# Performance work log

Hardware: AMD Instinct MI355X
Metric: run time of the kernel (lower is better)

The kernel has to match this reference:

```python
import jax, jax.numpy as jnp
import numpy as np

N = 100000      # nodes
E = 1600000     # edges (avg degree 16)
IN_DIM = 128
OUT_DIM = 64


def setup_inputs() -> dict:
    key = jax.random.key(0)
    k1, k2, k3, k4, k5 = jax.random.split(key, 5)
    h = jax.random.normal(k1, (N, IN_DIM), dtype=jnp.float32)
    W = jax.random.normal(k2, (IN_DIM, OUT_DIM), dtype=jnp.float32) * 0.05
    a = jax.random.normal(k3, (2 * OUT_DIM,), dtype=jnp.float32) * 0.05
    src = jax.random.randint(k4, (E,), 0, N, dtype=jnp.int32)
    dst = jax.random.randint(k5, (E,), 0, N, dtype=jnp.int32)
    return {"h": h, "W": W, "a": a, "src": src, "dst": dst}


def reference(h, W, a, src, dst):
    # z = W h  (node projection)
    z = h @ W                                   # [N, D]
    # Edge attention: e_ij = leaky_relu(a^T [z_i || z_j])
    # decomposed: a = [a_src; a_dst] -> e = leaky_relu(<z_src,a_src>+<z_dst,a_dst>)
    a_src, a_dst = a[:OUT_DIM], a[OUT_DIM:]
    s_src = z @ a_src                           # [N]
    s_dst = z @ a_dst                           # [N]
    e = jax.nn.leaky_relu(s_src[src] + s_dst[dst])  # [E], slope 0.01 (torch default)
    # Segmented softmax over incoming edges of each dst node
    m = jax.ops.segment_max(e, dst, num_segments=N)       # [N]
    m = jnp.where(jnp.isneginf(m), 0.0, m)                # empty mailboxes
    ex = jnp.exp(e - m[dst])                              # [E]
    denom = jax.ops.segment_sum(ex, dst, num_segments=N)  # [N]
    alpha = ex / jnp.where(denom == 0.0, 1.0, denom)[dst] # [E]
    # Weighted sum of source messages per dst node
    out = jax.ops.segment_sum(alpha[:, None] * z[src], dst, num_segments=N)  # [N, D]
    return out
```

## Files before the change

kernel.cpp:

```cpp
#include <hip/hip_runtime.h>
#include <math.h>

#define NN   100000
#define NE   1600000
#define IND  128
#define OUTD 64

#define BK_NODES 50
#define NBUCK    2000
#define CAPB     1024
#define CAPN     64

#define OFF_Z      0
#define OFF_SSRC   (OFF_Z + NN * OUTD / 2)
#define OFF_SDST   (OFF_SSRC + NN)
#define OFF_BCNT   (OFF_SDST + NN)
#define OFF_WSW    (OFF_BCNT + NBUCK)
#define OFF_COARSE (OFF_WSW + 4096)

typedef __bf16 bf16x8 __attribute__((ext_vector_type(8)));
typedef unsigned short u16x8 __attribute__((ext_vector_type(8)));
typedef float f32x4 __attribute__((ext_vector_type(4)));

union FragU { u16x8 u; bf16x8 b; };

__device__ __forceinline__ unsigned short f32_to_bf16_rne(float x)
{
    unsigned int b = __float_as_uint(x);
    b += 0x7FFFu + ((b >> 16) & 1u);
    return (unsigned short)(b >> 16);
}

#define WLPAD 136
#define ZTPAD 72

__global__ void __launch_bounds__(256) k_zs(
    const float* __restrict__ h, const unsigned short* __restrict__ wsw,
    const float* __restrict__ a, unsigned short* __restrict__ z16,
    float* __restrict__ s_src, float* __restrict__ s_dst)
{
    __shared__ __attribute__((aligned(16))) unsigned short HL[64 * WLPAD];
    int t = threadIdx.x;
    int base = blockIdx.x * 64;

    const float4* hg = reinterpret_cast<const float4*>(h);
#pragma unroll
    for (int i = 0; i < 8; ++i) {
        int idx = i * 256 + t;
        int r = idx >> 5;
        int c4 = idx & 31;
        float4 v = make_float4(0.f, 0.f, 0.f, 0.f);
        if (base + r < NN) v = hg[(base + r) * 32 + c4];
        unsigned int lo = (unsigned int)f32_to_bf16_rne(v.x) |
                          ((unsigned int)f32_to_bf16_rne(v.y) << 16);
        unsigned int hi = (unsigned int)f32_to_bf16_rne(v.z) |
                          ((unsigned int)f32_to_bf16_rne(v.w) << 16);
        *reinterpret_cast<uint2*>(&HL[r * WLPAD + c4 * 4]) = make_uint2(lo, hi);
    }

    int lane = t & 63;
    int wave = t >> 6;
    int c = lane & 15;
    int g = lane >> 4;

    FragU bf[4][4];
#pragma unroll
    for (int ks = 0; ks < 4; ++ks)
#pragma unroll
        for (int nt = 0; nt < 4; ++nt)
            bf[ks][nt].u = *reinterpret_cast<const u16x8*>(
                &wsw[((ks * 4 + nt) * 64 + lane) * 8]);

    __syncthreads();

    FragU af[4];
#pragma unroll
    for (int ks = 0; ks < 4; ++ks)
        af[ks].u = *reinterpret_cast<const u16x8*>(
            &HL[(wave * 16 + c) * WLPAD + ks * 32 + g * 8]);

    f32x4 acc[4];
#pragma unroll
    for (int nt = 0; nt < 4; ++nt) acc[nt] = (f32x4){0.f, 0.f, 0.f, 0.f};

#pragma unroll
    for (int nt = 0; nt < 4; ++nt)
#pragma unroll
        for (int ks = 0; ks < 4; ++ks)
            acc[nt] = __builtin_amdgcn_mfma_f32_16x16x32_bf16(
                af[ks].b, bf[ks][nt].b, acc[nt], 0, 0, 0);

    int rbase = base + wave * 16;
    float as[4], ad[4];
#pragma unroll
    for (int nt = 0; nt < 4; ++nt) {
        as[nt] = a[nt * 16 + c];
        ad[nt] = a[OUTD + nt * 16 + c];
    }

#pragma unroll
    for (int reg = 0; reg < 4; ++reg) {
        int row = rbase + g * 4 + reg;
        float p1 = 0.f, p2 = 0.f;
#pragma unroll
        for (int nt = 0; nt < 4; ++nt) {
            float v = acc[nt][reg];
            p1 = fmaf(v, as[nt], p1);
            p2 = fmaf(v, ad[nt], p2);
        }
#pragma unroll
        for (int mm = 1; mm < 16; mm <<= 1) {
            p1 += __shfl_xor(p1, mm, 64);
            p2 += __shfl_xor(p2, mm, 64);
        }
        if (c == 0 && row < NN) {
            s_src[row] = p1;
            s_dst[row] = p2;
        }
    }

    __syncthreads();
    unsigned short* ZT = HL;
    int zrow = wave * 16 + g * 4;
#pragma unroll
    for (int reg = 0; reg < 4; ++reg)
#pragma unroll
        for (int nt = 0; nt < 4; ++nt)
            ZT[(zrow + reg) * ZTPAD + nt * 16 + c] = f32_to_bf16_rne(acc[nt][reg]);
    __syncthreads();

#pragma unroll
    for (int i = 0; i < 2; ++i) {
        int j = i * 256 + t;
        int r = j >> 3;
        int c16 = j & 7;
        if (base + r < NN) {
            uint4 v = *reinterpret_cast<const uint4*>(&ZT[r * ZTPAD + c16 * 8]);
            *reinterpret_cast<uint4*>(&z16[(base + r) * OUTD + c16 * 8]) = v;
        }
    }
}

#define BIN_THREADS 1024
#define BIN_EPT     4
#define BIN_BLOCKS  391

__global__ void __launch_bounds__(BIN_THREADS) k_bin(
    const int* __restrict__ src, const int* __restrict__ dst,
    const float* __restrict__ W, unsigned short* __restrict__ wsw,
    int* __restrict__ bcnt, unsigned int* __restrict__ coarse)
{
    __shared__ int lhist[NBUCK];
    __shared__ int lbase[NBUCK];
    int t = threadIdx.x;

    if (blockIdx.x == 0) {
        int ks = t >> 8;
        int nt = (t >> 6) & 3;
        int lane = t & 63;
        int g = lane >> 4, c = lane & 15;
        u16x8 u;
#pragma unroll
        for (int j = 0; j < 8; ++j)
            u[j] = f32_to_bf16_rne(W[(ks * 32 + g * 8 + j) * OUTD + nt * 16 + c]);
        *reinterpret_cast<u16x8*>(&wsw[((ks * 4 + nt) * 64 + lane) * 8]) = u;
    }

    for (int i = t; i < NBUCK; i += BIN_THREADS) lhist[i] = 0;
    __syncthreads();

    int sv[BIN_EPT], dv[BIN_EPT];
    bool val[BIN_EPT];
#pragma unroll
    for (int i = 0; i < BIN_EPT; ++i) {
        int e = blockIdx.x * (BIN_THREADS * BIN_EPT) + i * BIN_THREADS + t;
        val[i] = e < NE;
        sv[i] = 0; dv[i] = 0;
        if (val[i]) { sv[i] = src[e]; dv[i] = dst[e]; }
    }
#pragma unroll
    for (int i = 0; i < BIN_EPT; ++i)
        if (val[i]) atomicAdd(&lhist[dv[i] / BK_NODES], 1);
    __syncthreads();

    for (int i = t; i < NBUCK; i += BIN_THREADS) {
        int c = lhist[i];
        lbase[i] = c ? atomicAdd(&bcnt[i], c) : 0;
        lhist[i] = 0;
    }
    __syncthreads();

#pragma unroll
    for (int i = 0; i < BIN_EPT; ++i) {
        if (val[i]) {
            int b = dv[i] / BK_NODES;
            int dl = dv[i] - b * BK_NODES;
            int r = atomicAdd(&lhist[b], 1);
            coarse[b * CAPB + lbase[b] + r] =
                ((unsigned int)sv[i] << 6) | (unsigned int)dl;
        }
    }
}

__global__ void __launch_bounds__(256) k_node(
    const unsigned short* __restrict__ z16, const unsigned int* __restrict__ coarse,
    const int* __restrict__ bcnt, const float* __restrict__ s_src,
    const float* __restrict__ s_dst, float* __restrict__ out)
{
    __shared__ unsigned int seg[BK_NODES * CAPN];
    __shared__ int cnt[BK_NODES];
    int b = blockIdx.x;
    int t = threadIdx.x;

    if (t < BK_NODES) cnt[t] = 0;
    __syncthreads();

    int nb = bcnt[b];
    if (nb > CAPB) nb = CAPB;
    const unsigned int* cb = coarse + b * CAPB;
    for (int i = t; i < nb; i += 256) {
        unsigned int v = cb[i];
        int dl = (int)(v & 63u);
        int s  = (int)(v >> 6);
        int r = atomicAdd(&cnt[dl], 1);
        if (r < CAPN) seg[dl * CAPN + r] = s;
    }
    __syncthreads();

    int wave = t >> 6;
    int lane = t & 63;
    int eslot = lane >> 4;
    int cbase = (lane & 15) * 4;

    for (int ni = wave; ni < BK_NODES; ni += 8) {
        int nj = ni + 4;
        bool hasB = (nj < BK_NODES);
        int nodeA = b * BK_NODES + ni;
        int nodeB = hasB ? (b * BK_NODES + nj) : nodeA;
        int dA = cnt[ni]; if (dA > CAPN) dA = CAPN;
        int dB = hasB ? cnt[nj] : 0; if (dB > CAPN) dB = CAPN;

        float sdstA = s_dst[nodeA];
        float sdstB = s_dst[nodeB];

        int sidA = 0, sidB = 0;
        float exA = 0.f, exB = 0.f;
        if (lane < dA) {
            sidA = (int)seg[ni * CAPN + lane];
            float e0 = s_src[sidA] + sdstA;
            exA = __expf(e0 > 0.f ? e0 : 0.01f * e0);
        }
        if (lane < dB) {
            sidB = (int)seg[nj * CAPN + lane];
            float e1 = s_src[sidB] + sdstB;
            exB = __expf(e1 > 0.f ? e1 : 0.01f * e1);
        }

        float lA = exA, lB = exB;
#pragma unroll
        for (int mm = 32; mm; mm >>= 1) {
            lA += __shfl_xor(lA, mm, 64);
            lB += __shfl_xor(lB, mm, 64);
        }
        int roA = sidA * OUTD;
        int roB = sidB * OUTD;

        float a0 = 0.f, a1 = 0.f, a2 = 0.f, a3 = 0.f;
        float c0 = 0.f, c1 = 0.f, c2 = 0.f, c3 = 0.f;
        int dmax = dA > dB ? dA : dB;
#pragma unroll 2
        for (int tt = 0; tt < dmax; tt += 4) {
            int e = tt + eslot;
            if (tt < dA) {
                int ro = __shfl(roA, e, 64);
                float exv = __shfl(exA, e, 64);
                uint2 v = *reinterpret_cast<const uint2*>(z16 + ro + cbase);
                a0 = fmaf(exv, __uint_as_float(v.x << 16), a0);
                a1 = fmaf(exv, __uint_as_float(v.x & 0xFFFF0000u), a1);
                a2 = fmaf(exv, __uint_as_float(v.y << 16), a2);
                a3 = fmaf(exv, __uint_as_float(v.y & 0xFFFF0000u), a3);
            }
            if (tt < dB) {
                int ro = __shfl(roB, e, 64);
                float exv = __shfl(exB, e, 64);
                uint2 v = *reinterpret_cast<const uint2*>(z16 + ro + cbase);
                c0 = fmaf(exv, __uint_as_float(v.x << 16), c0);
                c1 = fmaf(exv, __uint_as_float(v.x & 0xFFFF0000u), c1);
                c2 = fmaf(exv, __uint_as_float(v.y << 16), c2);
                c3 = fmaf(exv, __uint_as_float(v.y & 0xFFFF0000u), c3);
            }
        }

        a0 += __shfl_xor(a0, 16, 64); c0 += __shfl_xor(c0, 16, 64);
        a1 += __shfl_xor(a1, 16, 64); c1 += __shfl_xor(c1, 16, 64);
        a2 += __shfl_xor(a2, 16, 64); c2 += __shfl_xor(c2, 16, 64);
        a3 += __shfl_xor(a3, 16, 64); c3 += __shfl_xor(c3, 16, 64);
        a0 += __shfl_xor(a0, 32, 64); c0 += __shfl_xor(c0, 32, 64);
        a1 += __shfl_xor(a1, 32, 64); c1 += __shfl_xor(c1, 32, 64);
        a2 += __shfl_xor(a2, 32, 64); c2 += __shfl_xor(c2, 32, 64);
        a3 += __shfl_xor(a3, 32, 64); c3 += __shfl_xor(c3, 32, 64);

        if (eslot == 0) {
            float invA = dA ? 1.f / lA : 0.f;
            *reinterpret_cast<float4*>(out + nodeA * OUTD + cbase) =
                make_float4(a0 * invA, a1 * invA, a2 * invA, a3 * invA);
            if (hasB) {
                float invB = dB ? 1.f / lB : 0.f;
                *reinterpret_cast<float4*>(out + nodeB * OUTD + cbase) =
                    make_float4(c0 * invB, c1 * invB, c2 * invB, c3 * invB);
            }
        }
    }
}

extern "C" void kernel_launch(void* const* d_in, const int* in_sizes, int n_in,
                              void* d_out, int out_size, void* d_ws, size_t ws_size,
                              hipStream_t stream)
{
    const float* h   = (const float*)d_in[0];
    const float* W   = (const float*)d_in[1];
    const float* a   = (const float*)d_in[2];
    const int*   src = (const int*)d_in[3];
    const int*   dst = (const int*)d_in[4];
    float* out = (float*)d_out;

    int* ws_i = (int*)d_ws;

    unsigned short* z16 = (unsigned short*)(ws_i + OFF_Z);
    float* s_src  = (float*)(ws_i + OFF_SSRC);
    float* s_dst  = (float*)(ws_i + OFF_SDST);
    int*   bcnt   = ws_i + OFF_BCNT;
    unsigned short* wsw = (unsigned short*)(ws_i + OFF_WSW);
    unsigned int* coarse = (unsigned int*)(ws_i + OFF_COARSE);

    hipMemsetAsync(bcnt, 0, NBUCK * sizeof(int), stream);

    k_bin<<<BIN_BLOCKS, BIN_THREADS, 0, stream>>>(src, dst, W, wsw, bcnt, coarse);

    k_zs<<<(NN + 63) / 64, 256, 0, stream>>>(h, wsw, a, z16, s_src, s_dst);

    k_node<<<NBUCK, 256, 0, stream>>>(z16, coarse, bcnt, s_src, s_dst, out);
}
```

Measured before the change: 94.05 us.

## Compute edge exp weights during bucket scatter and store fp16 in LDS

Moves the per-edge attention score and exp computation from the per-node wave loop into the bucket scatter phase, where all 256 threads work over edges. The weights are stored as fp16 in shared memory, and the per-node denominator is accumulated with shared-memory float atomics. The gather loop then reads the source id and weight from LDS instead of using cross-lane shuffles. This balances the exp work across threads and removes the shuffle reductions. In exchange it adds LDS atomics and fp16 rounding of the weights, and the loop guard now uses e<dA per lane instead of tt<dA.

```diff
diff --git a/kernel.cpp b/kernel.cpp
--- a/kernel.cpp
+++ b/kernel.cpp
@@ -23,6 +23,7 @@
 typedef float f32x4 __attribute__((ext_vector_type(4)));
 
 union FragU { u16x8 u; bf16x8 b; };
+union HalfCv { unsigned short u; _Float16 f; };
 
 __device__ __forceinline__ unsigned short f32_to_bf16_rne(float x)
 {
@@ -208,11 +209,18 @@
     const float* __restrict__ s_dst, float* __restrict__ out)
 {
     __shared__ unsigned int seg[BK_NODES * CAPN];
+    __shared__ unsigned short exs[BK_NODES * CAPN];
+    __shared__ float lsum[BK_NODES];
+    __shared__ float sd[BK_NODES];
     __shared__ int cnt[BK_NODES];
     int b = blockIdx.x;
     int t = threadIdx.x;
 
-    if (t < BK_NODES) cnt[t] = 0;
+    if (t < BK_NODES) {
+        cnt[t] = 0;
+        lsum[t] = 0.f;
+        sd[t] = s_dst[b * BK_NODES + t];
+    }
     __syncthreads();
 
     int nb = bcnt[b];
@@ -222,8 +230,15 @@
         unsigned int v = cb[i];
         int dl = (int)(v & 63u);
         int s  = (int)(v >> 6);
+        float e0 = s_src[s] + sd[dl];
+        float ex = __expf(e0 > 0.f ? e0 : 0.01f * e0);
         int r = atomicAdd(&cnt[dl], 1);
-        if (r < CAPN) seg[dl * CAPN + r] = s;
+        if (r < CAPN) {
+            seg[dl * CAPN + r] = (unsigned int)s;
+            HalfCv cv; cv.f = (_Float16)ex;
+            exs[dl * CAPN + r] = cv.u;
+            atomicAdd(&lsum[dl], ex);
+        }
     }
     __syncthreads();
 
@@ -239,31 +254,8 @@
         int nodeB = hasB ? (b * BK_NODES + nj) : nodeA;
         int dA = cnt[ni]; if (dA > CAPN) dA = CAPN;
         int dB = hasB ? cnt[nj] : 0; if (dB > CAPN) dB = CAPN;
-
-        float sdstA = s_dst[nodeA];
-        float sdstB = s_dst[nodeB];
-
-        int sidA = 0, sidB = 0;
-        float exA = 0.f, exB = 0.f;
-        if (lane < dA) {
-            sidA = (int)seg[ni * CAPN + lane];
-            float e0 = s_src[sidA] + sdstA;
-            exA = __expf(e0 > 0.f ? e0 : 0.01f * e0);
-        }
-        if (lane < dB) {
-            sidB = (int)seg[nj * CAPN + lane];
-            float e1 = s_src[sidB] + sdstB;
-            exB = __expf(e1 > 0.f ? e1 : 0.01f * e1);
-        }
-
-        float lA = exA, lB = exB;
-#pragma unroll
-        for (int mm = 32; mm; mm >>= 1) {
-            lA += __shfl_xor(lA, mm, 64);
-            lB += __shfl_xor(lB, mm, 64);
-        }
-        int roA = sidA * OUTD;
-        int roB = sidB * OUTD;
+        float lA = lsum[ni];
+        float lB = hasB ? lsum[nj] : 1.f;
 
         float a0 = 0.f, a1 = 0.f, a2 = 0.f, a3 = 0.f;
         float c0 = 0.f, c1 = 0.f, c2 = 0.f, c3 = 0.f;
@@ -271,18 +263,20 @@
 #pragma unroll 2
         for (int tt = 0; tt < dmax; tt += 4) {
             int e = tt + eslot;
-            if (tt < dA) {
-                int ro = __shfl(roA, e, 64);
-                float exv = __shfl(exA, e, 64);
+            if (e < dA) {
+                int ro = (int)seg[ni * CAPN + e] * OUTD;
+                HalfCv cv; cv.u = exs[ni * CAPN + e];
+                float exv = (float)cv.f;
                 uint2 v = *reinterpret_cast<const uint2*>(z16 + ro + cbase);
                 a0 = fmaf(exv, __uint_as_float(v.x << 16), a0);
                 a1 = fmaf(exv, __uint_as_float(v.x & 0xFFFF0000u), a1);
                 a2 = fmaf(exv, __uint_as_float(v.y << 16), a2);
                 a3 = fmaf(exv, __uint_as_float(v.y & 0xFFFF0000u), a3);
             }
-            if (tt < dB) {
-                int ro = __shfl(roB, e, 64);
-                float exv = __shfl(exB, e, 64);
+            if (e < dB) {
+                int ro = (int)seg[nj * CAPN + e] * OUTD;
+                HalfCv cv; cv.u = exs[nj * CAPN + e];
+                float exv = (float)cv.f;
                 uint2 v = *reinterpret_cast<const uint2*>(z16 + ro + cbase);
                 c0 = fmaf(exv, __uint_as_float(v.x << 16), c0);
                 c1 = fmaf(exv, __uint_as_float(v.x & 0xFFFF0000u), c1);
```

New measurement: 95.14 us. Within noise of the previous version (+1.2%).

## Fuse edge binning and node projection into one interleaved kernel

Applied to the files above, without the earlier changes.

Merges the edge-bucketing kernel and the z/score projection kernel into a single launch. Every fifth block bins 4096 edges while the other four each project 64 nodes, so the latency-bound atomic scatter can overlap the compute-bound projection. A tiny init kernel now zeroes the bucket counters and swizzles W, replacing the memset and the block-0 special case. The shared buffer is reused between the two roles (16 KB for histograms fits within the 17 KB tile). Bin blocks now have 256 threads with 16 edges per thread, which puts more sequential atomic work on each thread.

```diff
diff --git a/kernel.cpp b/kernel.cpp
--- a/kernel.cpp
+++ b/kernel.cpp
@@ -31,17 +31,86 @@
     return (unsigned short)(b >> 16);
 }
 
+__global__ void __launch_bounds__(1024) k_init(
+    const float* __restrict__ W, unsigned short* __restrict__ wsw,
+    int* __restrict__ bcnt)
+{
+    int t = threadIdx.x;
+    for (int i = t; i < NBUCK; i += 1024) bcnt[i] = 0;
+
+    int ks = t >> 8;
+    int nt = (t >> 6) & 3;
+    int lane = t & 63;
+    int g = lane >> 4, c = lane & 15;
+    u16x8 u;
+#pragma unroll
+    for (int j = 0; j < 8; ++j)
+        u[j] = f32_to_bf16_rne(W[(ks * 32 + g * 8 + j) * OUTD + nt * 16 + c]);
+    *reinterpret_cast<u16x8*>(&wsw[((ks * 4 + nt) * 64 + lane) * 8]) = u;
+}
+
 #define WLPAD 136
 #define ZTPAD 72
-
-__global__ void __launch_bounds__(256) k_zs(
+#define PRE_BLOCKS 1955
+#define BIN_EPT    16
+
+__global__ void __launch_bounds__(256) k_pre(
     const float* __restrict__ h, const unsigned short* __restrict__ wsw,
-    const float* __restrict__ a, unsigned short* __restrict__ z16,
-    float* __restrict__ s_src, float* __restrict__ s_dst)
-{
-    __shared__ __attribute__((aligned(16))) unsigned short HL[64 * WLPAD];
+    const float* __restrict__ a, const int* __restrict__ src,
+    const int* __restrict__ dst, unsigned short* __restrict__ z16,
+    float* __restrict__ s_src, float* __restrict__ s_dst,
+    int* __restrict__ bcnt, unsigned int* __restrict__ coarse)
+{
+    __shared__ __attribute__((aligned(16))) unsigned char smem[64 * WLPAD * 2];
     int t = threadIdx.x;
-    int base = blockIdx.x * 64;
+    int grp = blockIdx.x / 5;
+    int o   = blockIdx.x % 5;
+
+    if (o == 4) {
+        int* lhist = reinterpret_cast<int*>(smem);
+        int* lbase = lhist + NBUCK;
+        int bin_id = grp;
+
+        for (int i = t; i < NBUCK; i += 256) lhist[i] = 0;
+        __syncthreads();
+
+        int sv[BIN_EPT], dv[BIN_EPT];
+        bool val[BIN_EPT];
+#pragma unroll
+        for (int i = 0; i < BIN_EPT; ++i) {
+            int e = bin_id * (256 * BIN_EPT) + i * 256 + t;
+            val[i] = e < NE;
+            sv[i] = 0; dv[i] = 0;
+            if (val[i]) { sv[i] = src[e]; dv[i] = dst[e]; }
+        }
+#pragma unroll
+        for (int i = 0; i < BIN_EPT; ++i)
+            if (val[i]) atomicAdd(&lhist[dv[i] / BK_NODES], 1);
+        __syncthreads();
+
+        for (int i = t; i < NBUCK; i += 256) {
+            int c = lhist[i];
+            lbase[i] = c ? atomicAdd(&bcnt[i], c) : 0;
+            lhist[i] = 0;
+        }
+        __syncthreads();
+
+#pragma unroll
+        for (int i = 0; i < BIN_EPT; ++i) {
+            if (val[i]) {
+                int b = dv[i] / BK_NODES;
+                int dl = dv[i] - b * BK_NODES;
+                int r = atomicAdd(&lhist[b], 1);
+                coarse[b * CAPB + lbase[b] + r] =
+                    ((unsigned int)sv[i] << 6) | (unsigned int)dl;
+            }
+        }
+        return;
+    }
+
+    unsigned short* HL = reinterpret_cast<unsigned short*>(smem);
+    int zs_id = grp * 4 + o;
+    int base = zs_id * 64;
 
     const float4* hg = reinterpret_cast<const float4*>(h);
 #pragma unroll
@@ -137,67 +206,6 @@
         if (base + r < NN) {
             uint4 v = *reinterpret_cast<const uint4*>(&ZT[r * ZTPAD + c16 * 8]);
             *reinterpret_cast<uint4*>(&z16[(base + r) * OUTD + c16 * 8]) = v;
-        }
-    }
-}
-
-#define BIN_THREADS 1024
-#define BIN_EPT     4
-#define BIN_BLOCKS  391
-
-__global__ void __launch_bounds__(BIN_THREADS) k_bin(
-    const int* __restrict__ src, const int* __restrict__ dst,
-    const float* __restrict__ W, unsigned short* __restrict__ wsw,
-    int* __restrict__ bcnt, unsigned int* __restrict__ coarse)
-{
-    __shared__ int lhist[NBUCK];
-    __shared__ int lbase[NBUCK];
-    int t = threadIdx.x;
-
-    if (blockIdx.x == 0) {
-        int ks = t >> 8;
-        int nt = (t >> 6) & 3;
-        int lane = t & 63;
-        int g = lane >> 4, c = lane & 15;
-        u16x8 u;
-#pragma unroll
-        for (int j = 0; j < 8; ++j)
-            u[j] = f32_to_bf16_rne(W[(ks * 32 + g * 8 + j) * OUTD + nt * 16 + c]);
-        *reinterpret_cast<u16x8*>(&wsw[((ks * 4 + nt) * 64 + lane) * 8]) = u;
-    }
-
-    for (int i = t; i < NBUCK; i += BIN_THREADS) lhist[i] = 0;
-    __syncthreads();
-
-    int sv[BIN_EPT], dv[BIN_EPT];
-    bool val[BIN_EPT];
-#pragma unroll
-    for (int i = 0; i < BIN_EPT; ++i) {
-        int e = blockIdx.x * (BIN_THREADS * BIN_EPT) + i * BIN_THREADS + t;
-        val[i] = e < NE;
-        sv[i] = 0; dv[i] = 0;
-        if (val[i]) { sv[i] = src[e]; dv[i] = dst[e]; }
-    }
-#pragma unroll
-    for (int i = 0; i < BIN_EPT; ++i)
-        if (val[i]) atomicAdd(&lhist[dv[i] / BK_NODES], 1);
-    __syncthreads();
-
-    for (int i = t; i < NBUCK; i += BIN_THREADS) {
-        int c = lhist[i];
-        lbase[i] = c ? atomicAdd(&bcnt[i], c) : 0;
-        lhist[i] = 0;
-    }
-    __syncthreads();
-
-#pragma unroll
-    for (int i = 0; i < BIN_EPT; ++i) {
-        if (val[i]) {
-            int b = dv[i] / BK_NODES;
-            int dl = dv[i] - b * BK_NODES;
-            int r = atomicAdd(&lhist[b], 1);
-            coarse[b * CAPB + lbase[b] + r] =
-                ((unsigned int)sv[i] << 6) | (unsigned int)dl;
         }
     }
 }
@@ -333,11 +341,10 @@
     unsigned short* wsw = (unsigned short*)(ws_i + OFF_WSW);
     unsigned int* coarse = (unsigned int*)(ws_i + OFF_COARSE);
 
-    hipMemsetAsync(bcnt, 0, NBUCK * sizeof(int), stream);
-
-    k_bin<<<BIN_BLOCKS, BIN_THREADS, 0, stream>>>(src, dst, W, wsw, bcnt, coarse);
-
-    k_zs<<<(NN + 63) / 64, 256, 0, stream>>>(h, wsw, a, z16, s_src, s_dst);
+    k_init<<<1, 1024, 0, stream>>>(W, wsw, bcnt);
+
+    k_pre<<<PRE_BLOCKS, 256, 0, stream>>>(h, wsw, a, src, dst, z16,
+                                          s_src, s_dst, bcnt, coarse);
 
     k_node<<<NBUCK, 256, 0, stream>>>(z16, coarse, bcnt, s_src, s_dst, out);
 }
```

Measured after the change: 89.94 us. 1.05x faster.
